# Kernel tuning notes

Hardware: AMD Instinct MI355X
Metric: run time of the kernel (lower is better)

## Reference

```python
import jax, jax.numpy as jnp
import numpy as np

N = 262144  # points
C = 256     # backbone_out_channels
K = 20      # semantic_num_classes
BN_EPS = 1e-3
EPS = 1e-8
IGNORE = -1


def setup_inputs() -> dict:
    key = jax.random.key(0)
    ks = jax.random.split(key, 12)
    feat = jax.random.normal(ks[0], (N, C), dtype=jnp.float32)
    coord = jax.random.normal(ks[1], (N, 3), dtype=jnp.float32)
    instance_centroid = jax.random.normal(ks[2], (N, 3), dtype=jnp.float32)
    segment = jax.random.randint(ks[3], (N,), 0, K, dtype=jnp.int32)
    instance = jax.random.randint(ks[4], (N,), 0, 1000, dtype=jnp.int32)
    # bias_head: Linear(C,C) -> BN1d(C) -> ReLU -> Linear(C,3)
    w1 = jax.random.normal(ks[5], (C, C), dtype=jnp.float32) * 0.02
    b1 = jnp.zeros((C,), dtype=jnp.float32)
    gamma = jnp.ones((C,), dtype=jnp.float32)
    beta = jnp.zeros((C,), dtype=jnp.float32)
    w2 = jax.random.normal(ks[6], (C, 3), dtype=jnp.float32) * 0.02
    b2 = jnp.zeros((3,), dtype=jnp.float32)
    # seg_head: Linear(C, K)
    ws = jax.random.normal(ks[7], (C, K), dtype=jnp.float32) * 0.02
    bs = jnp.zeros((K,), dtype=jnp.float32)
    return dict(feat=feat, coord=coord, instance_centroid=instance_centroid,
                segment=segment, instance=instance,
                w1=w1, b1=b1, gamma=gamma, beta=beta, w2=w2, b2=b2, ws=ws, bs=bs)


def reference(feat, coord, instance_centroid, segment, instance,
              w1, b1, gamma, beta, w2, b2, ws, bs):
    # bias head: Linear -> BatchNorm1d (training stats) -> ReLU -> Linear
    h = feat @ w1 + b1                                  # [N, C]
    mu = jnp.mean(h, axis=0)
    var = jnp.mean((h - mu) ** 2, axis=0)               # biased var (torch BN)
    h = (h - mu) * jax.lax.rsqrt(var + BN_EPS) * gamma + beta
    h = jax.nn.relu(h)
    bias_pred = h @ w2 + b2                             # [N, 3]

    logit_pred = feat @ ws + bs                         # [N, K]

    # semantic cross-entropy with ignore_index
    valid = segment != IGNORE
    tgt = jnp.where(valid, segment, 0)
    logp = jax.nn.log_softmax(logit_pred, axis=-1)
    nll = -jnp.take_along_axis(logp, tgt[:, None], axis=1)[:, 0]
    vf = valid.astype(logit_pred.dtype)
    seg_loss = jnp.sum(nll * vf) / (jnp.sum(vf) + EPS)

    # masked bias L1 loss
    mask = (instance != IGNORE).astype(bias_pred.dtype)
    bias_gt = instance_centroid - coord                 # [N, 3]
    bias_dist = jnp.sum(jnp.abs(bias_pred - bias_gt), axis=-1)
    msum = jnp.sum(mask) + EPS
    bias_l1_loss = jnp.sum(bias_dist * mask) / msum

    # masked cosine (direction) loss
    pred_n = bias_pred / (jnp.linalg.norm(bias_pred, axis=1, keepdims=True) + EPS)
    gt_n = bias_gt / (jnp.linalg.norm(bias_gt, axis=1, keepdims=True) + EPS)
    cos = -jnp.sum(pred_n * gt_n, axis=-1)
    bias_cosine_loss = jnp.sum(cos * mask) / msum

    loss = seg_loss + bias_l1_loss + bias_cosine_loss
    return jnp.stack([loss, seg_loss, bias_l1_loss, bias_cosine_loss])
```

## Files before the change

### kernel.cpp

```cpp
#include <hip/hip_runtime.h>
#include <cstdio>
#include <cstdint>

typedef unsigned int u32;
typedef unsigned short u16;
typedef short bf16x8 __attribute__((ext_vector_type(8)));
typedef float f32x4 __attribute__((ext_vector_type(4)));

#define NPTS 262144
#define CDIM 256
#define KCLS 20
#define NBLK 4096
#define NSLOT 256
#define LSLOT 256

#define OFF_WT    ((size_t)134217728)
#define OFF_W2T   (OFF_WT + (size_t)163840)
#define OFF_AGGBN (OFF_W2T + (size_t)8192)
#define OFF_AGGNL (OFF_AGGBN + (size_t)524288)
#define OFF_AGGL  (OFF_AGGNL + (size_t)2048)
#define OFF_AB    (OFF_AGGL + (size_t)4096)
#define WS_NEED   (OFF_AB + (size_t)2048)
#define MEMSET_OFF OFF_AGGBN
#define MEMSET_LEN ((size_t)(524288 + 2048 + 4096))

__device__ __forceinline__ u16 bf16rne(float x) {
    u32 u = __float_as_uint(x);
    u32 r = u + 0x7FFFu + ((u >> 16) & 1u);
    return (u16)(r >> 16);
}
__device__ __forceinline__ float bf2f(u16 b) {
    return __uint_as_float(((u32)b) << 16);
}

__global__ void k_prep(const float* __restrict__ w1, const float* __restrict__ wsm,
                       const float* __restrict__ w2,
                       u16* __restrict__ Wt2, u16* __restrict__ w2t) {
    int k = blockIdx.x;
    int n = threadIdx.x;
    float v = 0.f;
    if (n < 256) v = w1[k * 256 + n];
    else if (n < 256 + KCLS) v = wsm[k * KCLS + (n - 256)];
    Wt2[((size_t)(k >> 3) * 320 + n) * 8 + (k & 7)] = bf16rne(v);
    if (n < 16) w2t[n * 256 + k] = bf16rne((n < 3) ? w2[k * 3 + n] : 0.f);
}

__global__ __launch_bounds__(256) void k_gemm(
    const float* __restrict__ feat, const float* __restrict__ b1,
    const float* __restrict__ bs, const int* __restrict__ segment,
    const u16* __restrict__ Wt2, u16* __restrict__ h_out,
    float* __restrict__ aggBN, float* __restrict__ aggNLL)
{
    __shared__ uint4 smem4[2560];
    uint4* const As4 = smem4;
    uint4* const Bs4 = smem4 + 512;

    const int t = threadIdx.x;
    const int lane = t & 63;
    const int wv = t >> 6;
    const int q = lane >> 4;
    const int i16 = lane & 15;
    const int row0 = blockIdx.x * 64;
    const int slot = blockIdx.x & (NSLOT - 1);

    const f32x4 fz = {0.f, 0.f, 0.f, 0.f};
    f32x4 acc[4][4];
    f32x4 lacc[2];
#pragma unroll
    for (int r = 0; r < 4; ++r)
#pragma unroll
        for (int c = 0; c < 4; ++c) acc[r][c] = fz;
    lacc[0] = fz; lacc[1] = fz;

    const int sm = t >> 2;
    const int sq = t & 3;
    const float* fsrc = feat + (size_t)(row0 + sm) * 256 + sq * 8;
    const int wsl = sm ^ (sq << 2);
    const int As_slot0 = sq * 64 + wsl;
    const int As_slot1 = (sq + 4) * 64 + wsl;

    float4 f[4][4];
#pragma unroll
    for (int kc = 0; kc < 4; ++kc) {
        const float* p = fsrc + kc * 64;
        f[kc][0] = *(const float4*)(p);
        f[kc][1] = *(const float4*)(p + 4);
        f[kc][2] = *(const float4*)(p + 32);
        f[kc][3] = *(const float4*)(p + 36);
    }

#pragma unroll
    for (int kc = 0; kc < 4; ++kc) {
        {
            uint4 pk;
            pk.x = (u32)bf16rne(f[kc][0].x) | ((u32)bf16rne(f[kc][0].y) << 16);
            pk.y = (u32)bf16rne(f[kc][0].z) | ((u32)bf16rne(f[kc][0].w) << 16);
            pk.z = (u32)bf16rne(f[kc][1].x) | ((u32)bf16rne(f[kc][1].y) << 16);
            pk.w = (u32)bf16rne(f[kc][1].z) | ((u32)bf16rne(f[kc][1].w) << 16);
            As4[As_slot0] = pk;
            pk.x = (u32)bf16rne(f[kc][2].x) | ((u32)bf16rne(f[kc][2].y) << 16);
            pk.y = (u32)bf16rne(f[kc][2].z) | ((u32)bf16rne(f[kc][2].w) << 16);
            pk.z = (u32)bf16rne(f[kc][3].x) | ((u32)bf16rne(f[kc][3].y) << 16);
            pk.w = (u32)bf16rne(f[kc][3].z) | ((u32)bf16rne(f[kc][3].w) << 16);
            As4[As_slot1] = pk;
        }
#pragma unroll
        for (int i = 0; i < 4; ++i) {
            const u16* src0 = Wt2 + ((size_t)(kc * 8 + wv) * 320 + i * 64 + lane) * 8;
            u32* dst0 = (u32*)&Bs4[wv * 256 + i * 64];
            __builtin_amdgcn_global_load_lds(
                (const __attribute__((address_space(1))) u32*)src0,
                (__attribute__((address_space(3))) u32*)dst0, 16, 0, 0);
            const u16* src1 = Wt2 + ((size_t)(kc * 8 + wv + 4) * 320 + i * 64 + lane) * 8;
            u32* dst1 = (u32*)&Bs4[(wv + 4) * 256 + i * 64];
            __builtin_amdgcn_global_load_lds(
                (const __attribute__((address_space(1))) u32*)(src1),
                (__attribute__((address_space(3))) u32*)dst1, 16, 0, 0);
        }
        __syncthreads();

#pragma unroll
        for (int s = 0; s < 2; ++s) {
            const int kq = s * 4 + q;
            bf16x8 lbf[2];
#pragma unroll
            for (int x = 0; x < 2; ++x)
                lbf[x] = *(const bf16x8*)(Wt2 +
                    ((size_t)(kc * 8 + kq) * 320 + 256 + x * 16 + i16) * 8);
            bf16x8 bfr[4], af[4], la;
#pragma unroll
            for (int c = 0; c < 4; ++c)
                bfr[c] = *(const bf16x8*)&Bs4[kq * 256 + wv * 64 + c * 16 + i16];
#pragma unroll
            for (int r = 0; r < 4; ++r)
                af[r] = *(const bf16x8*)&As4[kq * 64 + ((r * 16 + i16) ^ (q << 2))];
            la = *(const bf16x8*)&As4[kq * 64 + ((wv * 16 + i16) ^ (q << 2))];

#pragma unroll
            for (int r = 0; r < 4; ++r)
#pragma unroll
                for (int c = 0; c < 4; ++c)
                    acc[r][c] = __builtin_amdgcn_mfma_f32_16x16x32_bf16(af[r], bfr[c], acc[r][c], 0, 0, 0);
#pragma unroll
            for (int x = 0; x < 2; ++x)
                lacc[x] = __builtin_amdgcn_mfma_f32_16x16x32_bf16(la, lbf[x], lacc[x], 0, 0, 0);
        }
        __syncthreads();
    }

    float b1v[4];
#pragma unroll
    for (int c = 0; c < 4; ++c) b1v[c] = b1[wv * 64 + c * 16 + i16];
    float bsv0 = bs[i16];
    float bsv1 = (16 + i16 < KCLS) ? bs[16 + i16] : 0.f;

    float nllacc = 0.f, cntacc = 0.f;
#pragma unroll
    for (int j = 0; j < 4; ++j) {
        int rowr = row0 + wv * 16 + q * 4 + j;
        float l0 = lacc[0][j] + bsv0;
        float l1raw = lacc[1][j] + bsv1;
        float l1m = (i16 < 4) ? l1raw : -3.0e38f;
        float mx = fmaxf(l0, l1m);
#pragma unroll
        for (int d = 1; d < 16; d <<= 1) mx = fmaxf(mx, __shfl_xor(mx, d));
        float s = __expf(l0 - mx) + ((i16 < 4) ? __expf(l1raw - mx) : 0.f);
#pragma unroll
        for (int d = 1; d < 16; d <<= 1) s += __shfl_xor(s, d);
        int tg = segment[rowr];
        float v0 = __shfl(l0, (lane & 48) + (tg & 15));
        float v1 = __shfl(l1raw, (lane & 48) + ((tg - 16) & 15));
        float lt = (tg < 16) ? v0 : v1;
        if (i16 == 0 && tg >= 0) {
            nllacc += __logf(s) + mx - lt;
            cntacc += 1.f;
        }
    }
#pragma unroll
    for (int d = 1; d < 64; d <<= 1) {
        nllacc += __shfl_xor(nllacc, d);
        cntacc += __shfl_xor(cntacc, d);
    }
    if (lane == 0) {
        atomicAdd(aggNLL + slot * 2 + 0, nllacc);
        atomicAdd(aggNLL + slot * 2 + 1, cntacc);
    }

#pragma unroll
    for (int c = 0; c < 4; ++c) {
        float s1 = 0.f, s2 = 0.f;
#pragma unroll
        for (int r = 0; r < 4; ++r)
#pragma unroll
            for (int j = 0; j < 4; ++j) {
                float v = acc[r][c][j] + b1v[c];
                s1 += v; s2 = fmaf(v, v, s2);
            }
        s1 += __shfl_xor(s1, 16); s1 += __shfl_xor(s1, 32);
        s2 += __shfl_xor(s2, 16); s2 += __shfl_xor(s2, 32);
        if (q == 0) {
            int ch = wv * 64 + c * 16 + i16;
            atomicAdd(aggBN + slot * 512 + ch, s1);
            atomicAdd(aggBN + slot * 512 + 256 + ch, s2);
        }
    }

    u16* Ht = (u16*)smem4;
#pragma unroll
    for (int r = 0; r < 4; ++r)
#pragma unroll
        for (int c = 0; c < 4; ++c)
#pragma unroll
            for (int j = 0; j < 4; ++j) {
                float v = acc[r][c][j] + b1v[c];
                int rw = r * 16 + q * 4 + j;
                int cl = wv * 64 + c * 16 + i16;
                Ht[rw * 264 + cl] = bf16rne(v);
            }
    __syncthreads();
#pragma unroll
    for (int i = 0; i < 8; ++i) {
        int c2 = i * 256 + t;
        int rb = c2 >> 9;
        int kc = (c2 >> 6) & 7;
        int qq = (c2 >> 4) & 3;
        int r16 = c2 & 15;
        uint4 v = *(const uint4*)((const char*)smem4 + (rb * 16 + r16) * 528 + kc * 64 + qq * 16);
        *(uint4*)((char*)h_out + (size_t)(blockIdx.x * 4 + rb) * 8192 + (size_t)(c2 & 511) * 16) = v;
    }
}

__global__ void k_reduce(const float* __restrict__ gamma, const float* __restrict__ beta,
                         const float* __restrict__ aggBN,
                         float* __restrict__ Aarr, float* __restrict__ Barr) {
    int c = blockIdx.x;
    int l = threadIdx.x;
    float s1 = 0.f, s2 = 0.f;
#pragma unroll
    for (int i = 0; i < 4; ++i) {
        int s = l + i * 64;
        s1 += aggBN[s * 512 + c];
        s2 += aggBN[s * 512 + 256 + c];
    }
#pragma unroll
    for (int d = 1; d < 64; d <<= 1) {
        s1 += __shfl_xor(s1, d);
        s2 += __shfl_xor(s2, d);
    }
    if (l == 0) {
        const float inv = 1.f / (float)NPTS;
        float mu = s1 * inv;
        float var = fmaxf(s2 * inv - mu * mu, 0.f);
        float a = gamma[c] * rsqrtf(var + 1e-3f);
        Aarr[c] = a;
        Barr[c] = beta[c] - mu * a;
    }
}

__global__ __launch_bounds__(256) void k_loss(
    const u16* __restrict__ h, const float* __restrict__ Aarr, const float* __restrict__ Barr,
    const u16* __restrict__ w2t, const float* __restrict__ b2,
    const float* __restrict__ coord, const float* __restrict__ cent,
    const int* __restrict__ inst, float* __restrict__ aggL)
{
    __shared__ float bp[4][16][4];
    __shared__ float red[12];

    const int t = threadIdx.x;
    const int lane = t & 63;
    const int wv = t >> 6;
    const int q = lane >> 4;
    const int i16 = lane & 15;
    const int row0 = blockIdx.x * 64;
    const int rb = blockIdx.x * 4 + wv;

    const u16* hb = h + (size_t)rb * 4096 + q * 128 + i16 * 8;
    bf16x8 hf[8];
#pragma unroll
    for (int kc = 0; kc < 8; ++kc)
        hf[kc] = *(const bf16x8*)(hb + kc * 512);

    bf16x8 wfr[8];
#pragma unroll
    for (int kc = 0; kc < 8; ++kc)
        wfr[kc] = *(const bf16x8*)(w2t + (size_t)i16 * 256 + kc * 32 + q * 8);
    float b2x = b2[0], b2y = b2[1], b2z = b2[2];

    const f32x4 fz = {0.f, 0.f, 0.f, 0.f};
    f32x4 c = fz;
#pragma unroll
    for (int kc = 0; kc < 8; ++kc) {
        float4 a0 = *(const float4*)(Aarr + kc * 32 + q * 8);
        float4 a1 = *(const float4*)(Aarr + kc * 32 + q * 8 + 4);
        float4 b0 = *(const float4*)(Barr + kc * 32 + q * 8);
        float4 b1 = *(const float4*)(Barr + kc * 32 + q * 8 + 4);
        float av[8] = {a0.x, a0.y, a0.z, a0.w, a1.x, a1.y, a1.z, a1.w};
        float bv[8] = {b0.x, b0.y, b0.z, b0.w, b1.x, b1.y, b1.z, b1.w};
        bf16x8 hn;
#pragma unroll
        for (int j = 0; j < 8; ++j) {
            float x = fmaxf(fmaf(bf2f(((const u16*)&hf[kc])[j]), av[j], bv[j]), 0.f);
            ((u16*)&hn)[j] = bf16rne(x);
        }
        c = __builtin_amdgcn_mfma_f32_16x16x32_bf16(hn, wfr[kc], c, 0, 0, 0);
    }

    if (i16 < 3) {
#pragma unroll
        for (int j = 0; j < 4; ++j) bp[wv][q * 4 + j][i16] = c[j];
    }
    float l1a = 0.f, cosa = 0.f, ma = 0.f;
    if (lane < 16) {
        int row = row0 + wv * 16 + lane;
        float4 P = *(const float4*)bp[wv][lane];
        float bpx = P.x + b2x, bpy = P.y + b2y, bpz = P.z + b2z;
        const float* cp = coord + (size_t)row * 3;
        const float* ip = cent + (size_t)row * 3;
        float gx = ip[0] - cp[0], gy = ip[1] - cp[1], gz = ip[2] - cp[2];
        float mk = (inst[row] != -1) ? 1.f : 0.f;
        float l1 = fabsf(bpx - gx) + fabsf(bpy - gy) + fabsf(bpz - gz);
        float np = sqrtf(fmaf(bpx, bpx, fmaf(bpy, bpy, bpz * bpz)));
        float ng = sqrtf(fmaf(gx, gx, fmaf(gy, gy, gz * gz)));
        float dp = fmaf(bpx, gx, fmaf(bpy, gy, bpz * gz));
        float cosv = -dp / ((np + 1e-8f) * (ng + 1e-8f));
        l1a = l1 * mk;
        cosa = cosv * mk;
        ma = mk;
    }
#pragma unroll
    for (int d = 1; d < 64; d <<= 1) {
        l1a += __shfl_xor(l1a, d);
        cosa += __shfl_xor(cosa, d);
        ma += __shfl_xor(ma, d);
    }
    if (lane == 0) { red[wv] = l1a; red[4 + wv] = cosa; red[8 + wv] = ma; }
    __syncthreads();
    if (t == 0) {
        int slot = blockIdx.x & (LSLOT - 1);
        atomicAdd(aggL + slot * 4 + 0, red[0] + red[1] + red[2] + red[3]);
        atomicAdd(aggL + slot * 4 + 1, red[4] + red[5] + red[6] + red[7]);
        atomicAdd(aggL + slot * 4 + 2, red[8] + red[9] + red[10] + red[11]);
    }
}

__global__ void k_final(const float* __restrict__ aggNLL, const float* __restrict__ aggL,
                        float* __restrict__ out) {
    int lane = threadIdx.x;
    float nll = 0.f, cnt = 0.f, l1 = 0.f, cs = 0.f, mk = 0.f;
#pragma unroll
    for (int i = 0; i < 4; ++i) {
        int s = lane + i * 64;
        nll += aggNLL[s * 2 + 0];
        cnt += aggNLL[s * 2 + 1];
        l1 += aggL[s * 4 + 0];
        cs += aggL[s * 4 + 1];
        mk += aggL[s * 4 + 2];
    }
#pragma unroll
    for (int d = 1; d < 64; d <<= 1) {
        nll += __shfl_xor(nll, d);
        cnt += __shfl_xor(cnt, d);
        l1 += __shfl_xor(l1, d);
        cs += __shfl_xor(cs, d);
        mk += __shfl_xor(mk, d);
    }
    if (lane == 0) {
        float seg = nll / (cnt + 1e-8f);
        float l1l = l1 / (mk + 1e-8f);
        float csl = cs / (mk + 1e-8f);
        out[0] = seg + l1l + csl;
        out[1] = seg;
        out[2] = l1l;
        out[3] = csl;
    }
}

extern "C" void kernel_launch(void* const* d_in, const int* in_sizes, int n_in,
                              void* d_out, int out_size, void* d_ws, size_t ws_size,
                              hipStream_t stream) {
    const float* feat   = (const float*)d_in[0];
    const float* coord  = (const float*)d_in[1];
    const float* cent   = (const float*)d_in[2];
    const int* segment  = (const int*)d_in[3];
    const int* inst     = (const int*)d_in[4];
    const float* w1     = (const float*)d_in[5];
    const float* b1     = (const float*)d_in[6];
    const float* gamma  = (const float*)d_in[7];
    const float* beta   = (const float*)d_in[8];
    const float* w2     = (const float*)d_in[9];
    const float* b2     = (const float*)d_in[10];
    const float* wsm    = (const float*)d_in[11];
    const float* bs     = (const float*)d_in[12];
    float* out = (float*)d_out;

    char* wsb = (char*)d_ws;
    u16* h_ws    = (u16*)wsb;
    u16* Wt2     = (u16*)(wsb + OFF_WT);
    u16* w2t     = (u16*)(wsb + OFF_W2T);
    float* aggBN = (float*)(wsb + OFF_AGGBN);
    float* aggNL = (float*)(wsb + OFF_AGGNL);
    float* aggL  = (float*)(wsb + OFF_AGGL);
    float* Aarr  = (float*)(wsb + OFF_AB);
    float* Barr  = Aarr + 256;

    if (ws_size < WS_NEED)
        fprintf(stderr, "kernel_launch: ws_size=%zu < needed %zu — WILL CORRUPT\n",
                ws_size, (size_t)WS_NEED);

    hipMemsetAsync(wsb + MEMSET_OFF, 0, MEMSET_LEN, stream);
    k_prep<<<256, 320, 0, stream>>>(w1, wsm, w2, Wt2, w2t);
    k_gemm<<<NBLK, 256, 0, stream>>>(feat, b1, bs, segment, Wt2, h_ws, aggBN, aggNL);
    k_reduce<<<256, 64, 0, stream>>>(gamma, beta, aggBN, Aarr, Barr);
    k_loss<<<4096, 256, 0, stream>>>(h_ws, Aarr, Barr, w2t, b2, coord, cent, inst, aggL);
    k_final<<<1, 64, 0, stream>>>(aggNL, aggL, out);
}
```

Baseline: 504.8 us.

## Keep full weight matrix resident in LDS with persistent 1024-thread GEMM blocks

Replaces the 4096-block tiled GEMM with 256 persistent 1024-thread blocks that load the whole bf16 W1+Ws matrix (144 KB) into LDS once. Each wave then processes 16-row strips straight from registers, with no A staging in shared memory and no per-k-chunk barriers. BN statistics are reduced in LDS and written once per block instead of through global atomics. The loss kernel now computes the 3-wide second linear layer with scalar FMAs over a strip-major h layout instead of an MFMA. In exchange, occupancy is limited to one block per CU, and there is less latency hiding for the feat loads.

```diff
diff --git a/kernel.cpp b/kernel.cpp
--- a/kernel.cpp
+++ b/kernel.cpp
@@ -10,13 +10,12 @@
 #define NPTS 262144
 #define CDIM 256
 #define KCLS 20
-#define NBLK 4096
-#define NSLOT 256
+#define NSTRIP 16384
 #define LSLOT 256
 
 #define OFF_WT    ((size_t)134217728)
-#define OFF_W2T   (OFF_WT + (size_t)163840)
-#define OFF_AGGBN (OFF_W2T + (size_t)8192)
+#define OFF_W2P   (OFF_WT + (size_t)163840)
+#define OFF_AGGBN (OFF_W2P + (size_t)8192)
 #define OFF_AGGNL (OFF_AGGBN + (size_t)524288)
 #define OFF_AGGL  (OFF_AGGNL + (size_t)2048)
 #define OFF_AB    (OFF_AGGL + (size_t)4096)
@@ -35,198 +34,141 @@
 
 __global__ void k_prep(const float* __restrict__ w1, const float* __restrict__ wsm,
                        const float* __restrict__ w2,
-                       u16* __restrict__ Wt2, u16* __restrict__ w2t) {
+                       u16* __restrict__ Wt3, float* __restrict__ w2p) {
     int k = blockIdx.x;
     int n = threadIdx.x;
     float v = 0.f;
     if (n < 256) v = w1[k * 256 + n];
     else if (n < 256 + KCLS) v = wsm[k * KCLS + (n - 256)];
-    Wt2[((size_t)(k >> 3) * 320 + n) * 8 + (k & 7)] = bf16rne(v);
-    if (n < 16) w2t[n * 256 + k] = bf16rne((n < 3) ? w2[k * 3 + n] : 0.f);
-}
-
-__global__ __launch_bounds__(256) void k_gemm(
+    int ct = n >> 4, i16 = n & 15;
+    int kq = k >> 5, q = (k >> 3) & 3, e = k & 7;
+    Wt3[(((size_t)(ct * 8 + kq) * 64) + (q * 16 + i16)) * 8 + e] = bf16rne(v);
+    if (n < 4) w2p[k * 4 + n] = (n < 3) ? w2[k * 3 + n] : 0.f;
+}
+
+__global__ __launch_bounds__(1024, 4) void k_fused(
     const float* __restrict__ feat, const float* __restrict__ b1,
     const float* __restrict__ bs, const int* __restrict__ segment,
-    const u16* __restrict__ Wt2, u16* __restrict__ h_out,
+    const u16* __restrict__ Wt3, u16* __restrict__ h2,
     float* __restrict__ aggBN, float* __restrict__ aggNLL)
 {
-    __shared__ uint4 smem4[2560];
-    uint4* const As4 = smem4;
-    uint4* const Bs4 = smem4 + 512;
+    __shared__ u16 W[73728];
+    __shared__ float bn[512];
+    __shared__ float nllw[2];
 
     const int t = threadIdx.x;
     const int lane = t & 63;
     const int wv = t >> 6;
     const int q = lane >> 4;
     const int i16 = lane & 15;
-    const int row0 = blockIdx.x * 64;
-    const int slot = blockIdx.x & (NSLOT - 1);
-
+
+    if (t < 512) bn[t] = 0.f;
+    if (t < 2) nllw[t] = 0.f;
+
+#pragma unroll
+    for (int j = 0; j < 9; ++j) {
+        int slab = wv * 9 + j;
+        const u16* src = Wt3 + (size_t)slab * 512 + lane * 8;
+        __builtin_amdgcn_global_load_lds(
+            (const __attribute__((address_space(1))) u32*)src,
+            (__attribute__((address_space(3))) u32*)&W[slab * 512], 16, 0, 0);
+    }
+    __syncthreads();
+
+    const float bsv0 = bs[i16];
+    const float bsv1 = (16 + i16 < KCLS) ? bs[16 + i16] : 0.f;
+    float nllacc = 0.f, cntacc = 0.f;
     const f32x4 fz = {0.f, 0.f, 0.f, 0.f};
-    f32x4 acc[4][4];
-    f32x4 lacc[2];
-#pragma unroll
-    for (int r = 0; r < 4; ++r)
-#pragma unroll
-        for (int c = 0; c < 4; ++c) acc[r][c] = fz;
-    lacc[0] = fz; lacc[1] = fz;
-
-    const int sm = t >> 2;
-    const int sq = t & 3;
-    const float* fsrc = feat + (size_t)(row0 + sm) * 256 + sq * 8;
-    const int wsl = sm ^ (sq << 2);
-    const int As_slot0 = sq * 64 + wsl;
-    const int As_slot1 = (sq + 4) * 64 + wsl;
-
-    float4 f[4][4];
-#pragma unroll
-    for (int kc = 0; kc < 4; ++kc) {
-        const float* p = fsrc + kc * 64;
-        f[kc][0] = *(const float4*)(p);
-        f[kc][1] = *(const float4*)(p + 4);
-        f[kc][2] = *(const float4*)(p + 32);
-        f[kc][3] = *(const float4*)(p + 36);
-    }
-
-#pragma unroll
-    for (int kc = 0; kc < 4; ++kc) {
-        {
-            uint4 pk;
-            pk.x = (u32)bf16rne(f[kc][0].x) | ((u32)bf16rne(f[kc][0].y) << 16);
-            pk.y = (u32)bf16rne(f[kc][0].z) | ((u32)bf16rne(f[kc][0].w) << 16);
-            pk.z = (u32)bf16rne(f[kc][1].x) | ((u32)bf16rne(f[kc][1].y) << 16);
-            pk.w = (u32)bf16rne(f[kc][1].z) | ((u32)bf16rne(f[kc][1].w) << 16);
-            As4[As_slot0] = pk;
-            pk.x = (u32)bf16rne(f[kc][2].x) | ((u32)bf16rne(f[kc][2].y) << 16);
-            pk.y = (u32)bf16rne(f[kc][2].z) | ((u32)bf16rne(f[kc][2].w) << 16);
-            pk.z = (u32)bf16rne(f[kc][3].x) | ((u32)bf16rne(f[kc][3].y) << 16);
-            pk.w = (u32)bf16rne(f[kc][3].z) | ((u32)bf16rne(f[kc][3].w) << 16);
-            As4[As_slot1] = pk;
-        }
-#pragma unroll
-        for (int i = 0; i < 4; ++i) {
-            const u16* src0 = Wt2 + ((size_t)(kc * 8 + wv) * 320 + i * 64 + lane) * 8;
-            u32* dst0 = (u32*)&Bs4[wv * 256 + i * 64];
-            __builtin_amdgcn_global_load_lds(
-                (const __attribute__((address_space(1))) u32*)src0,
-                (__attribute__((address_space(3))) u32*)dst0, 16, 0, 0);
-            const u16* src1 = Wt2 + ((size_t)(kc * 8 + wv + 4) * 320 + i * 64 + lane) * 8;
-            u32* dst1 = (u32*)&Bs4[(wv + 4) * 256 + i * 64];
-            __builtin_amdgcn_global_load_lds(
-                (const __attribute__((address_space(1))) u32*)(src1),
-                (__attribute__((address_space(3))) u32*)dst1, 16, 0, 0);
-        }
-        __syncthreads();
-
-#pragma unroll
-        for (int s = 0; s < 2; ++s) {
-            const int kq = s * 4 + q;
-            bf16x8 lbf[2];
-#pragma unroll
-            for (int x = 0; x < 2; ++x)
-                lbf[x] = *(const bf16x8*)(Wt2 +
-                    ((size_t)(kc * 8 + kq) * 320 + 256 + x * 16 + i16) * 8);
-            bf16x8 bfr[4], af[4], la;
-#pragma unroll
-            for (int c = 0; c < 4; ++c)
-                bfr[c] = *(const bf16x8*)&Bs4[kq * 256 + wv * 64 + c * 16 + i16];
-#pragma unroll
-            for (int r = 0; r < 4; ++r)
-                af[r] = *(const bf16x8*)&As4[kq * 64 + ((r * 16 + i16) ^ (q << 2))];
-            la = *(const bf16x8*)&As4[kq * 64 + ((wv * 16 + i16) ^ (q << 2))];
-
-#pragma unroll
-            for (int r = 0; r < 4; ++r)
-#pragma unroll
-                for (int c = 0; c < 4; ++c)
-                    acc[r][c] = __builtin_amdgcn_mfma_f32_16x16x32_bf16(af[r], bfr[c], acc[r][c], 0, 0, 0);
-#pragma unroll
-            for (int x = 0; x < 2; ++x)
-                lacc[x] = __builtin_amdgcn_mfma_f32_16x16x32_bf16(la, lbf[x], lacc[x], 0, 0, 0);
-        }
-        __syncthreads();
-    }
-
-    float b1v[4];
-#pragma unroll
-    for (int c = 0; c < 4; ++c) b1v[c] = b1[wv * 64 + c * 16 + i16];
-    float bsv0 = bs[i16];
-    float bsv1 = (16 + i16 < KCLS) ? bs[16 + i16] : 0.f;
-
-    float nllacc = 0.f, cntacc = 0.f;
-#pragma unroll
-    for (int j = 0; j < 4; ++j) {
-        int rowr = row0 + wv * 16 + q * 4 + j;
-        float l0 = lacc[0][j] + bsv0;
-        float l1raw = lacc[1][j] + bsv1;
-        float l1m = (i16 < 4) ? l1raw : -3.0e38f;
-        float mx = fmaxf(l0, l1m);
-#pragma unroll
-        for (int d = 1; d < 16; d <<= 1) mx = fmaxf(mx, __shfl_xor(mx, d));
-        float s = __expf(l0 - mx) + ((i16 < 4) ? __expf(l1raw - mx) : 0.f);
-#pragma unroll
-        for (int d = 1; d < 16; d <<= 1) s += __shfl_xor(s, d);
-        int tg = segment[rowr];
-        float v0 = __shfl(l0, (lane & 48) + (tg & 15));
-        float v1 = __shfl(l1raw, (lane & 48) + ((tg - 16) & 15));
-        float lt = (tg < 16) ? v0 : v1;
-        if (i16 == 0 && tg >= 0) {
-            nllacc += __logf(s) + mx - lt;
-            cntacc += 1.f;
-        }
-    }
+
+#pragma unroll 1
+    for (int i = 0; i < 4; ++i) {
+        const int s = blockIdx.x * 64 + i * 16 + wv;
+        const float* fb = feat + (size_t)(s * 16 + i16) * 256 + q * 8;
+        float4 fA[8], fB[8];
+#pragma unroll
+        for (int kq = 0; kq < 8; ++kq) {
+            fA[kq] = *(const float4*)(fb + kq * 32);
+            fB[kq] = *(const float4*)(fb + kq * 32 + 4);
+        }
+        bf16x8 af[8];
+#pragma unroll
+        for (int kq = 0; kq < 8; ++kq) {
+            bf16x8 f;
+            ((u16*)&f)[0] = bf16rne(fA[kq].x); ((u16*)&f)[1] = bf16rne(fA[kq].y);
+            ((u16*)&f)[2] = bf16rne(fA[kq].z); ((u16*)&f)[3] = bf16rne(fA[kq].w);
+            ((u16*)&f)[4] = bf16rne(fB[kq].x); ((u16*)&f)[5] = bf16rne(fB[kq].y);
+            ((u16*)&f)[6] = bf16rne(fB[kq].z); ((u16*)&f)[7] = bf16rne(fB[kq].w);
+            af[kq] = f;
+        }
+
+#pragma unroll
+        for (int ct = 0; ct < 16; ++ct) {
+            f32x4 a = fz;
+#pragma unroll
+            for (int kq = 0; kq < 8; ++kq)
+                a = __builtin_amdgcn_mfma_f32_16x16x32_bf16(
+                    af[kq], *(const bf16x8*)&W[((ct * 8 + kq) * 64 + lane) * 8], a, 0, 0, 0);
+            float b1v = b1[ct * 16 + i16];
+            float v0 = a[0] + b1v, v1 = a[1] + b1v, v2 = a[2] + b1v, v3 = a[3] + b1v;
+            u32 d0 = (u32)bf16rne(v0) | ((u32)bf16rne(v1) << 16);
+            u32 d1 = (u32)bf16rne(v2) | ((u32)bf16rne(v3) << 16);
+            uint2 dd = {d0, d1};
+            *(uint2*)((char*)h2 + (size_t)s * 8192 + ct * 512 + lane * 8) = dd;
+            float s1 = v0 + v1 + v2 + v3;
+            float s2 = fmaf(v0, v0, fmaf(v1, v1, fmaf(v2, v2, v3 * v3)));
+            s1 += __shfl_xor(s1, 16); s1 += __shfl_xor(s1, 32);
+            s2 += __shfl_xor(s2, 16); s2 += __shfl_xor(s2, 32);
+            if (lane < 16) {
+                atomicAdd(&bn[ct * 16 + lane], s1);
+                atomicAdd(&bn[256 + ct * 16 + lane], s2);
+            }
+        }
+
+        f32x4 l0 = fz, l1 = fz;
+#pragma unroll
+        for (int kq = 0; kq < 8; ++kq) {
+            l0 = __builtin_amdgcn_mfma_f32_16x16x32_bf16(
+                af[kq], *(const bf16x8*)&W[((16 * 8 + kq) * 64 + lane) * 8], l0, 0, 0, 0);
+            l1 = __builtin_amdgcn_mfma_f32_16x16x32_bf16(
+                af[kq], *(const bf16x8*)&W[((17 * 8 + kq) * 64 + lane) * 8], l1, 0, 0, 0);
+        }
+#pragma unroll
+        for (int j = 0; j < 4; ++j) {
+            int rowr = s * 16 + q * 4 + j;
+            float a0 = l0[j] + bsv0;
+            float a1raw = l1[j] + bsv1;
+            float a1m = (i16 < 4) ? a1raw : -3.0e38f;
+            float mx = fmaxf(a0, a1m);
+#pragma unroll
+            for (int d = 1; d < 16; d <<= 1) mx = fmaxf(mx, __shfl_xor(mx, d));
+            float se = __expf(a0 - mx) + ((i16 < 4) ? __expf(a1raw - mx) : 0.f);
+#pragma unroll
+            for (int d = 1; d < 16; d <<= 1) se += __shfl_xor(se, d);
+            int tg = segment[rowr];
+            float v0 = __shfl(a0, (lane & 48) + (tg & 15));
+            float v1 = __shfl(a1raw, (lane & 48) + ((tg - 16) & 15));
+            float lt = (tg < 16) ? v0 : v1;
+            if (i16 == 0 && tg >= 0) {
+                nllacc += __logf(se) + mx - lt;
+                cntacc += 1.f;
+            }
+        }
+    }
+
 #pragma unroll
     for (int d = 1; d < 64; d <<= 1) {
         nllacc += __shfl_xor(nllacc, d);
         cntacc += __shfl_xor(cntacc, d);
     }
     if (lane == 0) {
-        atomicAdd(aggNLL + slot * 2 + 0, nllacc);
-        atomicAdd(aggNLL + slot * 2 + 1, cntacc);
-    }
-
-#pragma unroll
-    for (int c = 0; c < 4; ++c) {
-        float s1 = 0.f, s2 = 0.f;
-#pragma unroll
-        for (int r = 0; r < 4; ++r)
-#pragma unroll
-            for (int j = 0; j < 4; ++j) {
-                float v = acc[r][c][j] + b1v[c];
-                s1 += v; s2 = fmaf(v, v, s2);
-            }
-        s1 += __shfl_xor(s1, 16); s1 += __shfl_xor(s1, 32);
-        s2 += __shfl_xor(s2, 16); s2 += __shfl_xor(s2, 32);
-        if (q == 0) {
-            int ch = wv * 64 + c * 16 + i16;
-            atomicAdd(aggBN + slot * 512 + ch, s1);
-            atomicAdd(aggBN + slot * 512 + 256 + ch, s2);
-        }
-    }
-
-    u16* Ht = (u16*)smem4;
-#pragma unroll
-    for (int r = 0; r < 4; ++r)
-#pragma unroll
-        for (int c = 0; c < 4; ++c)
-#pragma unroll
-            for (int j = 0; j < 4; ++j) {
-                float v = acc[r][c][j] + b1v[c];
-                int rw = r * 16 + q * 4 + j;
-                int cl = wv * 64 + c * 16 + i16;
-                Ht[rw * 264 + cl] = bf16rne(v);
-            }
+        atomicAdd(&nllw[0], nllacc);
+        atomicAdd(&nllw[1], cntacc);
+    }
     __syncthreads();
-#pragma unroll
-    for (int i = 0; i < 8; ++i) {
-        int c2 = i * 256 + t;
-        int rb = c2 >> 9;
-        int kc = (c2 >> 6) & 7;
-        int qq = (c2 >> 4) & 3;
-        int r16 = c2 & 15;
-        uint4 v = *(const uint4*)((const char*)smem4 + (rb * 16 + r16) * 528 + kc * 64 + qq * 16);
-        *(uint4*)((char*)h_out + (size_t)(blockIdx.x * 4 + rb) * 8192 + (size_t)(c2 & 511) * 16) = v;
+    if (t < 512) aggBN[(size_t)blockIdx.x * 512 + t] = bn[t];
+    if (t == 0) {
+        aggNLL[blockIdx.x * 2 + 0] = nllw[0];
+        aggNLL[blockIdx.x * 2 + 1] = nllw[1];
     }
 }
 
@@ -258,12 +200,11 @@
 }
 
 __global__ __launch_bounds__(256) void k_loss(
-    const u16* __restrict__ h, const float* __restrict__ Aarr, const float* __restrict__ Barr,
-    const u16* __restrict__ w2t, const float* __restrict__ b2,
+    const u16* __restrict__ h2, const float* __restrict__ Aarr, const float* __restrict__ Barr,
+    const float* __restrict__ w2p, const float* __restrict__ b2,
     const float* __restrict__ coord, const float* __restrict__ cent,
     const int* __restrict__ inst, float* __restrict__ aggL)
 {
-    __shared__ float bp[4][16][4];
     __shared__ float red[12];
 
     const int t = threadIdx.x;
@@ -271,68 +212,62 @@
     const int wv = t >> 6;
     const int q = lane >> 4;
     const int i16 = lane & 15;
-    const int row0 = blockIdx.x * 64;
-    const int rb = blockIdx.x * 4 + wv;
-
-    const u16* hb = h + (size_t)rb * 4096 + q * 128 + i16 * 8;
-    bf16x8 hf[8];
-#pragma unroll
-    for (int kc = 0; kc < 8; ++kc)
-        hf[kc] = *(const bf16x8*)(hb + kc * 512);
-
-    bf16x8 wfr[8];
-#pragma unroll
-    for (int kc = 0; kc < 8; ++kc)
-        wfr[kc] = *(const bf16x8*)(w2t + (size_t)i16 * 256 + kc * 32 + q * 8);
-    float b2x = b2[0], b2y = b2[1], b2z = b2[2];
-
-    const f32x4 fz = {0.f, 0.f, 0.f, 0.f};
-    f32x4 c = fz;
-#pragma unroll
-    for (int kc = 0; kc < 8; ++kc) {
-        float4 a0 = *(const float4*)(Aarr + kc * 32 + q * 8);
-        float4 a1 = *(const float4*)(Aarr + kc * 32 + q * 8 + 4);
-        float4 b0 = *(const float4*)(Barr + kc * 32 + q * 8);
-        float4 b1 = *(const float4*)(Barr + kc * 32 + q * 8 + 4);
-        float av[8] = {a0.x, a0.y, a0.z, a0.w, a1.x, a1.y, a1.z, a1.w};
-        float bv[8] = {b0.x, b0.y, b0.z, b0.w, b1.x, b1.y, b1.z, b1.w};
-        bf16x8 hn;
-#pragma unroll
-        for (int j = 0; j < 8; ++j) {
-            float x = fmaxf(fmaf(bf2f(((const u16*)&hf[kc])[j]), av[j], bv[j]), 0.f);
-            ((u16*)&hn)[j] = bf16rne(x);
-        }
-        c = __builtin_amdgcn_mfma_f32_16x16x32_bf16(hn, wfr[kc], c, 0, 0, 0);
-    }
-
-    if (i16 < 3) {
-#pragma unroll
-        for (int j = 0; j < 4; ++j) bp[wv][q * 4 + j][i16] = c[j];
-    }
+    const int s = blockIdx.x * 4 + wv;
+
+    float px[4] = {0.f, 0.f, 0.f, 0.f};
+    float py[4] = {0.f, 0.f, 0.f, 0.f};
+    float pz[4] = {0.f, 0.f, 0.f, 0.f};
+
+#pragma unroll
+    for (int ct = 0; ct < 16; ++ct) {
+        uint2 d = *(const uint2*)((const char*)h2 + (size_t)s * 8192 + ct * 512 + lane * 8);
+        int ch = ct * 16 + i16;
+        float A = Aarr[ch], B = Barr[ch];
+        float4 w = *(const float4*)(w2p + ch * 4);
+        float hv[4] = {bf2f((u16)(d.x & 0xffff)), bf2f((u16)(d.x >> 16)),
+                       bf2f((u16)(d.y & 0xffff)), bf2f((u16)(d.y >> 16))};
+#pragma unroll
+        for (int j = 0; j < 4; ++j) {
+            float v = fmaxf(fmaf(hv[j], A, B), 0.f);
+            px[j] = fmaf(v, w.x, px[j]);
+            py[j] = fmaf(v, w.y, py[j]);
+            pz[j] = fmaf(v, w.z, pz[j]);
+        }
+    }
+#pragma unroll
+    for (int d = 1; d < 16; d <<= 1) {
+#pragma unroll
+        for (int j = 0; j < 4; ++j) {
+            px[j] += __shfl_xor(px[j], d);
+            py[j] += __shfl_xor(py[j], d);
+            pz[j] += __shfl_xor(pz[j], d);
+        }
+    }
+
     float l1a = 0.f, cosa = 0.f, ma = 0.f;
-    if (lane < 16) {
-        int row = row0 + wv * 16 + lane;
-        float4 P = *(const float4*)bp[wv][lane];
-        float bpx = P.x + b2x, bpy = P.y + b2y, bpz = P.z + b2z;
-        const float* cp = coord + (size_t)row * 3;
-        const float* ip = cent + (size_t)row * 3;
-        float gx = ip[0] - cp[0], gy = ip[1] - cp[1], gz = ip[2] - cp[2];
-        float mk = (inst[row] != -1) ? 1.f : 0.f;
-        float l1 = fabsf(bpx - gx) + fabsf(bpy - gy) + fabsf(bpz - gz);
-        float np = sqrtf(fmaf(bpx, bpx, fmaf(bpy, bpy, bpz * bpz)));
-        float ng = sqrtf(fmaf(gx, gx, fmaf(gy, gy, gz * gz)));
-        float dp = fmaf(bpx, gx, fmaf(bpy, gy, bpz * gz));
-        float cosv = -dp / ((np + 1e-8f) * (ng + 1e-8f));
-        l1a = l1 * mk;
-        cosa = cosv * mk;
-        ma = mk;
-    }
-#pragma unroll
-    for (int d = 1; d < 64; d <<= 1) {
-        l1a += __shfl_xor(l1a, d);
-        cosa += __shfl_xor(cosa, d);
-        ma += __shfl_xor(ma, d);
-    }
+    if (i16 == 0) {
+        float b2x = b2[0], b2y = b2[1], b2z = b2[2];
+#pragma unroll
+        for (int j = 0; j < 4; ++j) {
+            int row = s * 16 + q * 4 + j;
+            float bpx = px[j] + b2x, bpy = py[j] + b2y, bpz = pz[j] + b2z;
+            const float* cp = coord + (size_t)row * 3;
+            const float* ip = cent + (size_t)row * 3;
+            float gx = ip[0] - cp[0], gy = ip[1] - cp[1], gz = ip[2] - cp[2];
+            float mk = (inst[row] != -1) ? 1.f : 0.f;
+            float l1 = fabsf(bpx - gx) + fabsf(bpy - gy) + fabsf(bpz - gz);
+            float np = sqrtf(fmaf(bpx, bpx, fmaf(bpy, bpy, bpz * bpz)));
+            float ng = sqrtf(fmaf(gx, gx, fmaf(gy, gy, gz * gz)));
+            float dp = fmaf(bpx, gx, fmaf(bpy, gy, bpz * gz));
+            float cosv = -dp / ((np + 1e-8f) * (ng + 1e-8f));
+            l1a += l1 * mk;
+            cosa += cosv * mk;
+            ma += mk;
+        }
+    }
+    l1a += __shfl_xor(l1a, 16); l1a += __shfl_xor(l1a, 32);
+    cosa += __shfl_xor(cosa, 16); cosa += __shfl_xor(cosa, 32);
+    ma += __shfl_xor(ma, 16); ma += __shfl_xor(ma, 32);
     if (lane == 0) { red[wv] = l1a; red[4 + wv] = cosa; red[8 + wv] = ma; }
     __syncthreads();
     if (t == 0) {
@@ -394,9 +329,9 @@
     float* out = (float*)d_out;
 
     char* wsb = (char*)d_ws;
-    u16* h_ws    = (u16*)wsb;
-    u16* Wt2     = (u16*)(wsb + OFF_WT);
-    u16* w2t     = (u16*)(wsb + OFF_W2T);
+    u16* h2      = (u16*)wsb;
+    u16* Wt3     = (u16*)(wsb + OFF_WT);
+    float* w2p   = (float*)(wsb + OFF_W2P);
     float* aggBN = (float*)(wsb + OFF_AGGBN);
     float* aggNL = (float*)(wsb + OFF_AGGNL);
     float* aggL  = (float*)(wsb + OFF_AGGL);
@@ -408,9 +343,9 @@
                 ws_size, (size_t)WS_NEED);
 
     hipMemsetAsync(wsb + MEMSET_OFF, 0, MEMSET_LEN, stream);
-    k_prep<<<256, 320, 0, stream>>>(w1, wsm, w2, Wt2, w2t);
-    k_gemm<<<NBLK, 256, 0, stream>>>(feat, b1, bs, segment, Wt2, h_ws, aggBN, aggNL);
+    k_prep<<<256, 288, 0, stream>>>(w1, wsm, w2, Wt3, w2p);
+    k_fused<<<256, 1024, 0, stream>>>(feat, b1, bs, segment, Wt3, h2, aggBN, aggNL);
     k_reduce<<<256, 64, 0, stream>>>(gamma, beta, aggBN, Aarr, Barr);
-    k_loss<<<4096, 256, 0, stream>>>(h_ws, Aarr, Barr, w2t, b2, coord, cent, inst, aggL);
+    k_loss<<<4096, 256, 0, stream>>>(h2, Aarr, Barr, w2p, b2, coord, cent, inst, aggL);
     k_final<<<1, 64, 0, stream>>>(aggNL, aggL, out);
 }
```

After: 1.129 ms. +123.7%, slower.
